# Optimization experiments

Hardware: AMD Instinct MI355X
Metric: run time of the kernel (lower is better)

Reference implementation:

```python
import jax, jax.numpy as jnp
import numpy as np


def setup_inputs() -> dict:
    key = jax.random.key(0)
    k1, k2 = jax.random.split(key)
    lut = jax.random.normal(k1, (1, 3, 33, 33, 33), dtype=jnp.float32)
    x = jax.random.uniform(k2, (8, 3, 1024, 1024), dtype=jnp.float32)
    return {"lut": lut, "x": x}


def reference(lut, x):
    # lut: [1, 3, D, D, D]; x: [B, 3, H, W] in [0,1]
    D = lut.shape[-1]
    lut0 = lut[0]  # [3, D, D, D], broadcast over batch (lut batch == 1)

    v = jnp.clip(x, 0.0, 1.0) * (D - 1)            # [B, 3, H, W]
    v = jnp.transpose(v, (0, 2, 3, 1))             # [B, H, W, 3]
    i0 = jnp.floor(v).astype(jnp.int32)            # [B, H, W, 3]
    i1 = jnp.minimum(i0 + 1, D - 1)
    f = v - i0.astype(v.dtype)                     # fractional part

    r0, g0, b0 = i0[..., 0], i0[..., 1], i0[..., 2]
    r1, g1, b1 = i1[..., 0], i1[..., 1], i1[..., 2]
    fr, fg, fb = f[..., 0], f[..., 1], f[..., 2]

    def gather(rr, gg, bb):
        # lut0[:, rr, gg, bb] -> [3, B, H, W] -> [B, 3, H, W]
        return jnp.transpose(lut0[:, rr, gg, bb], (1, 0, 2, 3))

    c000 = gather(r0, g0, b0)
    c100 = gather(r1, g0, b0)
    c010 = gather(r0, g1, b0)
    c110 = gather(r1, g1, b0)
    c001 = gather(r0, g0, b1)
    c101 = gather(r1, g0, b1)
    c011 = gather(r0, g1, b1)
    c111 = gather(r1, g1, b1)

    one = jnp.float32(1.0)
    w000 = ((one - fr) * (one - fg) * (one - fb))[:, None]
    w100 = (fr * (one - fg) * (one - fb))[:, None]
    w010 = ((one - fr) * fg * (one - fb))[:, None]
    w110 = (fr * fg * (one - fb))[:, None]
    w001 = ((one - fr) * (one - fg) * fb)[:, None]
    w101 = (fr * (one - fg) * fb)[:, None]
    w011 = ((one - fr) * fg * fb)[:, None]
    w111 = (fr * fg * fb)[:, None]

    out = (c000 * w000 + c100 * w100 + c010 * w010 + c110 * w110 +
           c001 * w001 + c101 * w101 + c011 * w011 + c111 * w111)
    return out  # [B, 3, H, W]
```

## Files before the change

### kernel.cpp

```cpp
#include <hip/hip_runtime.h>


#define D   33
#define D2  (33 * 33)
#define D3  (33 * 33 * 33)
#define NP  (D3 - 1)
#define HW  (1024 * 1024)
#define QHW (HW / 4)
#define NG  (8 * QHW)
#define CHUNKS 256
#define GPC (NG / CHUNKS)
#define THREADS 1024
#define ITERS (GPC / THREADS)
#define PAIRS (ITERS / 2)

typedef __fp16 h16;
typedef __attribute__((ext_vector_type(2))) __fp16 h16x2;
typedef __attribute__((ext_vector_type(4))) float f32x4;

#define DOT2(a, b) __builtin_amdgcn_fdot2((a), (b), 0.0f, false)

__global__ __launch_bounds__(THREADS) void lut3d_kernel(
    const float* __restrict__ lut, const float* __restrict__ x,
    float* __restrict__ out)
{
    const int c     = blockIdx.x;
    const int chunk = blockIdx.y;

    __shared__ h16x2 ls[NP];
    {
        const float* lc = lut + c * D3;
        for (int i = threadIdx.x; i < NP; i += THREADS) {
            h16x2 v;
            v.x = (h16)lc[i];
            v.y = (h16)lc[i + 1];
            ls[i] = v;
        }
    }
    __syncthreads();

    const int tid  = threadIdx.x;
    const int base = chunk * GPC;
    const int bidx = base >> 18;
    const int pb   = (base & (QHW - 1)) * 4;

    const float* xp = x   + (size_t)bidx * 3 * HW + pb;
    float*       op = out + (size_t)bidx * 3 * HW + (size_t)c * HW + pb;

    auto do_group = [&](int fo, float4 xr, float4 xg, float4 xB) {
        const float rr[4] = {xr.x, xr.y, xr.z, xr.w};
        const float gg[4] = {xg.x, xg.y, xg.z, xg.w};
        const float bb[4] = {xB.x, xB.y, xB.z, xB.w};
        float oo[4];
        #pragma unroll
        for (int j = 0; j < 4; ++j) {
            const float vr = fminf(fmaxf(rr[j], 0.f) * 32.f, 31.999998f);
            const float vg = fminf(fmaxf(gg[j], 0.f) * 32.f, 31.999998f);
            const float vb = fminf(fmaxf(bb[j], 0.f) * 32.f, 31.999998f);

            const int r0 = (int)vr, g0 = (int)vg, b0 = (int)vb;
            const float fb = vb - (float)b0;
            const float fg = vg - (float)g0;
            const float fr = vr - (float)r0;

            const int idx = __mul24(r0, D2) + __mul24(g0, D) + b0;

            const h16x2 h00 = ls[idx];
            const h16x2 h01 = ls[idx + D];
            const h16x2 h10 = ls[idx + D2];
            const h16x2 h11 = ls[idx + D2 + D];

            const h16x2 w = __builtin_amdgcn_cvt_pkrtz(1.0f - fb, fb);
            const float c00 = DOT2(h00, w);
            const float c01 = DOT2(h01, w);
            const float c10 = DOT2(h10, w);
            const float c11 = DOT2(h11, w);

            const float cg0 = c00 + fg * (c01 - c00);
            const float cg1 = c10 + fg * (c11 - c10);
            oo[j] = cg0 + fr * (cg1 - cg0);
        }
        f32x4 ov;
        ov.x = oo[0]; ov.y = oo[1]; ov.z = oo[2]; ov.w = oo[3];
        __builtin_nontemporal_store(ov, (f32x4*)(op + fo));
    };

    float4 a0, a1, a2, b0, b1, b2;
    {
        const int f0 = tid * 4;
        const int f1 = f0 + THREADS * 4;
        a0 = *(const float4*)(xp + f0);
        a1 = *(const float4*)(xp + f0 + HW);
        a2 = *(const float4*)(xp + f0 + 2 * HW);
        b0 = *(const float4*)(xp + f1);
        b1 = *(const float4*)(xp + f1 + HW);
        b2 = *(const float4*)(xp + f1 + 2 * HW);
    }

    #pragma unroll 1
    for (int pr = 0; pr < PAIRS; ++pr) {
        float4 n0, n1, n2, m0, m1, m2;
        if (pr + 1 < PAIRS) {
            const int f0 = (2 * (pr + 1)) * (THREADS * 4) + tid * 4;
            const int f1 = f0 + THREADS * 4;
            n0 = *(const float4*)(xp + f0);
            n1 = *(const float4*)(xp + f0 + HW);
            n2 = *(const float4*)(xp + f0 + 2 * HW);
            m0 = *(const float4*)(xp + f1);
            m1 = *(const float4*)(xp + f1 + HW);
            m2 = *(const float4*)(xp + f1 + 2 * HW);
        }
        const int fo0 = (2 * pr) * (THREADS * 4) + tid * 4;
        do_group(fo0,                a0, a1, a2);
        do_group(fo0 + THREADS * 4,  b0, b1, b2);
        a0 = n0; a1 = n1; a2 = n2;
        b0 = m0; b1 = m1; b2 = m2;
    }
}

extern "C" void kernel_launch(void* const* d_in, const int* in_sizes, int n_in,
                              void* d_out, int out_size, void* d_ws, size_t ws_size,
                              hipStream_t stream) {
    const float* lut = (const float*)d_in[0];
    const float* x   = (const float*)d_in[1];
    float* out = (float*)d_out;

    dim3 grid(3, CHUNKS);
    lut3d_kernel<<<grid, THREADS, 0, stream>>>(lut, x, out);
}
```

Baseline: 225.8 us.

## Halve LUT shared memory with scalar fp16 table, drop prefetch pipeline for occupancy

The shared LUT now holds single fp16 values (about 70KB) instead of overlapping fp16 pairs (about 140KB), and each pair is assembled from two 16-bit LDS reads. The aim is to fit more blocks per CU, and launch bounds now request a minimum of 8. The software prefetch of the next two groups is replaced by a simple one-group-per-iteration loop to cut register pressure. The nontemporal output store becomes a plain store. In exchange the kernel issues twice as many LDS reads per corner, loses explicit load/compute overlap, and the output store may now pollute the cache.

```diff
diff --git a/kernel.cpp b/kernel.cpp
--- a/kernel.cpp
+++ b/kernel.cpp
@@ -4,40 +4,33 @@
 #define D   33
 #define D2  (33 * 33)
 #define D3  (33 * 33 * 33)
-#define NP  (D3 - 1)
 #define HW  (1024 * 1024)
 #define QHW (HW / 4)
-#define NG  (8 * QHW)
 #define CHUNKS 256
-#define GPC (NG / CHUNKS)
+#define GPC ((8 * QHW) / CHUNKS)
 #define THREADS 1024
 #define ITERS (GPC / THREADS)
-#define PAIRS (ITERS / 2)
 
 typedef __fp16 h16;
 typedef __attribute__((ext_vector_type(2))) __fp16 h16x2;
-typedef __attribute__((ext_vector_type(4))) float f32x4;
 
 #define DOT2(a, b) __builtin_amdgcn_fdot2((a), (b), 0.0f, false)
 
-__global__ __launch_bounds__(THREADS) void lut3d_kernel(
+__global__ __launch_bounds__(THREADS, 8) void lut3d_kernel(
     const float* __restrict__ lut, const float* __restrict__ x,
     float* __restrict__ out)
 {
     const int c     = blockIdx.x;
     const int chunk = blockIdx.y;
 
-    __shared__ h16x2 ls[NP];
+    __shared__ h16 ls[D3];
     {
         const float* lc = lut + c * D3;
-        for (int i = threadIdx.x; i < NP; i += THREADS) {
-            h16x2 v;
-            v.x = (h16)lc[i];
-            v.y = (h16)lc[i + 1];
-            ls[i] = v;
-        }
+        for (int i = threadIdx.x; i < D3; i += THREADS) ls[i] = (h16)lc[i];
     }
     __syncthreads();
+
+    const unsigned short* lu = (const unsigned short*)ls;
 
     const int tid  = threadIdx.x;
     const int base = chunk * GPC;
@@ -47,11 +40,19 @@
     const float* xp = x   + (size_t)bidx * 3 * HW + pb;
     float*       op = out + (size_t)bidx * 3 * HW + (size_t)c * HW + pb;
 
-    auto do_group = [&](int fo, float4 xr, float4 xg, float4 xB) {
+    #pragma unroll 1
+    for (int it = 0; it < ITERS; ++it) {
+        const int fo = it * (THREADS * 4) + tid * 4;
+
+        const float4 xr = *(const float4*)(xp + fo);
+        const float4 xg = *(const float4*)(xp + fo + HW);
+        const float4 xB = *(const float4*)(xp + fo + 2 * HW);
+
         const float rr[4] = {xr.x, xr.y, xr.z, xr.w};
         const float gg[4] = {xg.x, xg.y, xg.z, xg.w};
         const float bb[4] = {xB.x, xB.y, xB.z, xB.w};
         float oo[4];
+
         #pragma unroll
         for (int j = 0; j < 4; ++j) {
             const float vr = fminf(fmaxf(rr[j], 0.f) * 32.f, 31.999998f);
@@ -65,56 +66,25 @@
 
             const int idx = __mul24(r0, D2) + __mul24(g0, D) + b0;
 
-            const h16x2 h00 = ls[idx];
-            const h16x2 h01 = ls[idx + D];
-            const h16x2 h10 = ls[idx + D2];
-            const h16x2 h11 = ls[idx + D2 + D];
+            const h16x2 w = __builtin_amdgcn_cvt_pkrtz(1.0f - fb, fb);
 
-            const h16x2 w = __builtin_amdgcn_cvt_pkrtz(1.0f - fb, fb);
-            const float c00 = DOT2(h00, w);
-            const float c01 = DOT2(h01, w);
-            const float c10 = DOT2(h10, w);
-            const float c11 = DOT2(h11, w);
+            auto cpair = [&](int i) -> float {
+                const unsigned int p = (unsigned int)lu[i]
+                                     | ((unsigned int)lu[i + 1] << 16);
+                return DOT2(__builtin_bit_cast(h16x2, p), w);
+            };
+
+            const float c00 = cpair(idx);
+            const float c01 = cpair(idx + D);
+            const float c10 = cpair(idx + D2);
+            const float c11 = cpair(idx + D2 + D);
 
             const float cg0 = c00 + fg * (c01 - c00);
             const float cg1 = c10 + fg * (c11 - c10);
             oo[j] = cg0 + fr * (cg1 - cg0);
         }
-        f32x4 ov;
-        ov.x = oo[0]; ov.y = oo[1]; ov.z = oo[2]; ov.w = oo[3];
-        __builtin_nontemporal_store(ov, (f32x4*)(op + fo));
-    };
 
-    float4 a0, a1, a2, b0, b1, b2;
-    {
-        const int f0 = tid * 4;
-        const int f1 = f0 + THREADS * 4;
-        a0 = *(const float4*)(xp + f0);
-        a1 = *(const float4*)(xp + f0 + HW);
-        a2 = *(const float4*)(xp + f0 + 2 * HW);
-        b0 = *(const float4*)(xp + f1);
-        b1 = *(const float4*)(xp + f1 + HW);
-        b2 = *(const float4*)(xp + f1 + 2 * HW);
-    }
-
-    #pragma unroll 1
-    for (int pr = 0; pr < PAIRS; ++pr) {
-        float4 n0, n1, n2, m0, m1, m2;
-        if (pr + 1 < PAIRS) {
-            const int f0 = (2 * (pr + 1)) * (THREADS * 4) + tid * 4;
-            const int f1 = f0 + THREADS * 4;
-            n0 = *(const float4*)(xp + f0);
-            n1 = *(const float4*)(xp + f0 + HW);
-            n2 = *(const float4*)(xp + f0 + 2 * HW);
-            m0 = *(const float4*)(xp + f1);
-            m1 = *(const float4*)(xp + f1 + HW);
-            m2 = *(const float4*)(xp + f1 + 2 * HW);
-        }
-        const int fo0 = (2 * pr) * (THREADS * 4) + tid * 4;
-        do_group(fo0,                a0, a1, a2);
-        do_group(fo0 + THREADS * 4,  b0, b1, b2);
-        a0 = n0; a1 = n1; a2 = n2;
-        b0 = m0; b1 = m1; b2 = m2;
+        *(float4*)(op + fo) = make_float4(oo[0], oo[1], oo[2], oo[3]);
     }
 }
 
```

Result: slower. 303.1 us (+34.2%).
